# Kernel tuning notes

Measured on AMD Instinct MI355X. Metric: run time of the kernel, lower is better.

## Reference

```python
import jax, jax.numpy as jnp
import numpy as np

N_NODES = 50000
N_EDGES = 800000
IN_DIM = 128
OUT_DIM = 128
NEG_SLOPE = 0.01  # F.leaky_relu default


def setup_inputs() -> dict:
    key = jax.random.key(0)
    k_h, k_src, k_dst, k_w, k_as, k_ad = jax.random.split(key, 6)
    h = jax.random.normal(k_h, (N_NODES, IN_DIM), dtype=jnp.float32)
    src = jax.random.randint(k_src, (N_EDGES,), 0, N_NODES, dtype=jnp.int32)
    dst = jax.random.randint(k_dst, (N_EDGES,), 0, N_NODES, dtype=jnp.int32)
    # fc weight: xavier_normal with relu gain; stored as [in, out] for h @ W
    gain = float(np.sqrt(2.0))
    std_w = gain * np.sqrt(2.0 / (IN_DIM + OUT_DIM))
    W = jax.random.normal(k_w, (IN_DIM, OUT_DIM), dtype=jnp.float32) * std_w
    # attn weight [1, 2*out] split into src/dst halves (concat@a == z_s@a_s + z_d@a_d)
    std_a = gain * np.sqrt(2.0 / (2 * OUT_DIM + 1))
    a_src = jax.random.normal(k_as, (OUT_DIM,), dtype=jnp.float32) * std_a
    a_dst = jax.random.normal(k_ad, (OUT_DIM,), dtype=jnp.float32) * std_a
    return {"h": h, "src": src, "dst": dst, "W": W, "a_src": a_src, "a_dst": a_dst}


def reference(h, src, dst, W, a_src, a_dst):
    n = h.shape[0]
    z = h @ W                                   # [N, D]
    # edge attention: leaky_relu(attn(concat[z_src, z_dst]))
    e = z[src] @ a_src + z[dst] @ a_dst         # [E]
    e = jnp.where(e >= 0, e, NEG_SLOPE * e)
    # segment softmax over incoming edges of each dst node
    m = jax.ops.segment_max(e, dst, num_segments=n)    # [N]
    m = jnp.where(jnp.isfinite(m), m, 0.0)             # guard zero-in-degree nodes
    ex = jnp.exp(e - m[dst])                            # [E]
    denom = jax.ops.segment_sum(ex, dst, num_segments=n)
    denom = jnp.where(denom > 0, denom, 1.0)
    alpha = ex / denom[dst]                             # [E]
    # weighted scatter-sum of source features
    out = jax.ops.segment_sum(alpha[:, None] * z[src], dst, num_segments=n)  # [N, D]
    return out
```

## Files before the change

kernel.cpp:

```cpp
#include <hip/hip_runtime.h>
#include <math.h>

#define DIM 128
#define NEG_SLOPE 0.01f
#define CAP 64
#define NFILL 1024

typedef __attribute__((ext_vector_type(8))) short bf16x8;
typedef __attribute__((ext_vector_type(4))) float f32x4;
typedef unsigned int uint;
typedef unsigned short ushort;

static __device__ __forceinline__ uint f2bf(float x) {
  uint u = __float_as_uint(x);
  return (u + 0x7fffu + ((u >> 16) & 1u)) >> 16;
}

__global__ __launch_bounds__(256) void prep2(
    const float* __restrict__ W,
    const float* __restrict__ a_src, const float* __restrict__ a_dst,
    const float* __restrict__ h,
    ushort* __restrict__ Wt16, float* __restrict__ s, float* __restrict__ d,
    int* __restrict__ cur, int n, int nsd)
{
  const int t = threadIdx.x;
  const int b = blockIdx.x;
  if (b == 0) {
    const float4* W4 = (const float4*)W;
    #pragma unroll
    for (int it = 0; it < 16; ++it) {
      int i = t + it * 256;
      int k = i >> 5, n4 = (i & 31) * 4;
      float4 v = W4[i];
      Wt16[(n4 + 0) * 128 + k] = (ushort)f2bf(v.x);
      Wt16[(n4 + 1) * 128 + k] = (ushort)f2bf(v.y);
      Wt16[(n4 + 2) * 128 + k] = (ushort)f2bf(v.z);
      Wt16[(n4 + 3) * 128 + k] = (ushort)f2bf(v.w);
    }
  } else if (b <= nsd) {
    __shared__ float vec[2][DIM];
    {
      const float* row = W + (size_t)(t & 127) * DIM;
      const float* a = (t < 128) ? a_src : a_dst;
      float acc = 0.f;
      #pragma unroll 16
      for (int j = 0; j < DIM; ++j) acc = fmaf(row[j], a[j], acc);
      vec[t >> 7][t & 127] = acc;
    }
    __syncthreads();
    int i = (b - 1) * 256 + t;
    if (i < n) {
      const float4* h4 = (const float4*)(h + (size_t)i * DIM);
      float sp = 0.f, dp = 0.f;
      #pragma unroll 8
      for (int c = 0; c < 32; ++c) {
        float4 v = h4[c];
        sp = fmaf(v.x, vec[0][c*4+0], fmaf(v.y, vec[0][c*4+1],
             fmaf(v.z, vec[0][c*4+2], fmaf(v.w, vec[0][c*4+3], sp))));
        dp = fmaf(v.x, vec[1][c*4+0], fmaf(v.y, vec[1][c*4+1],
             fmaf(v.z, vec[1][c*4+2], fmaf(v.w, vec[1][c*4+3], dp))));
      }
      s[i] = sp; d[i] = dp;
    }
  } else {
    int i = (b - 1 - nsd) * 256 + t;
    if (i < n) cur[i] = i * CAP;
  }
}

__global__ __launch_bounds__(256) void gemm_mfma(
    const float* __restrict__ h, const ushort* __restrict__ Wt16,
    uint* __restrict__ zb,
    int n)
{
  __shared__ __align__(16) ushort hb[64 * 136];
  __shared__ __align__(16) ushort Wt[128 * 136];

  const int t = threadIdx.x;
  const int lane = t & 63, wv = t >> 6;
  const int row0 = blockIdx.x * 64;

  {
    const float4* h4 = (const float4*)h;
    #pragma unroll
    for (int it = 0; it < 8; ++it) {
      int i = t + it * 256;
      int r = i >> 5, c4 = i & 31;
      float4 v = make_float4(0.f, 0.f, 0.f, 0.f);
      if (row0 + r < n) v = h4[(size_t)(row0 + r) * 32 + c4];
      uint2 pk;
      pk.x = f2bf(v.x) | (f2bf(v.y) << 16);
      pk.y = f2bf(v.z) | (f2bf(v.w) << 16);
      *(uint2*)&hb[r * 136 + c4 * 4] = pk;
    }
  }
  {
    const uint4* Wg = (const uint4*)Wt16;
    #pragma unroll
    for (int it = 0; it < 8; ++it) {
      int i = t + it * 256;
      int nn = i >> 4, k8 = (i & 15) * 8;
      *(uint4*)&Wt[nn * 136 + k8] = Wg[i];
    }
  }
  __syncthreads();

  f32x4 acc[8];
  #pragma unroll
  for (int c = 0; c < 8; ++c) acc[c] = (f32x4){0.f, 0.f, 0.f, 0.f};

  const int m = lane & 15, quad = lane >> 4;
  const ushort* arow = &hb[(wv * 16 + m) * 136 + quad * 8];
  const ushort* brow = &Wt[m * 136 + quad * 8];

  #pragma unroll
  for (int ks = 0; ks < 4; ++ks) {
    bf16x8 af = *(const bf16x8*)(arow + ks * 32);
    #pragma unroll
    for (int c = 0; c < 8; ++c) {
      bf16x8 bf = *(const bf16x8*)(brow + c * 16 * 136 + ks * 32);
      acc[c] = __builtin_amdgcn_mfma_f32_16x16x32_bf16(af, bf, acc[c], 0, 0, 0);
    }
  }

  __syncthreads();
  #pragma unroll
  for (int c = 0; c < 8; ++c) {
    int col = c * 16 + m;
    #pragma unroll
    for (int reg = 0; reg < 4; ++reg) {
      int r = wv * 16 + quad * 4 + reg;
      hb[r * 136 + col] = (ushort)f2bf(acc[c][reg]);
    }
  }
  __syncthreads();
  #pragma unroll
  for (int it = 0; it < 4; ++it) {
    int i = t + it * 256;
    int r = i >> 4, c8 = i & 15;
    int rg = row0 + r;
    if (rg < n) {
      uint4 v = *(uint4*)&hb[r * 136 + c8 * 8];
      *(uint4*)&zb[(size_t)rg * 64 + c8 * 4] = v;
    }
  }
}

__global__ __launch_bounds__(256) void fill_bucket(
    const int* __restrict__ src, const int* __restrict__ dst,
    const float* __restrict__ s, const float* __restrict__ d,
    int* __restrict__ cur, uint* __restrict__ bucket, int E)
{
  const int base = blockIdx.x * 256 + threadIdx.x;
  const int stride = NFILL * 256;

  int idx[4]; bool ok[4];
  #pragma unroll
  for (int u = 0; u < 4; ++u) {
    int i = base + u * stride;
    ok[u] = (i < E);
    idx[u] = ok[u] ? i : 0;
  }
  int sj[4], dj[4];
  #pragma unroll
  for (int u = 0; u < 4; ++u) sj[u] = src[idx[u]];
  #pragma unroll
  for (int u = 0; u < 4; ++u) dj[u] = dst[idx[u]];
  float sv[4], dv[4];
  #pragma unroll
  for (int u = 0; u < 4; ++u) sv[u] = s[sj[u]];
  #pragma unroll
  for (int u = 0; u < 4; ++u) dv[u] = d[dj[u]];

  uint rec[4];
  #pragma unroll
  for (int u = 0; u < 4; ++u) {
    float e = sv[u] + dv[u];
    e = (e >= 0.f) ? e : NEG_SLOPE * e;
    rec[u] = (uint)sj[u] | (f2bf(__expf(e)) << 16);
  }
  int p[4];
  #pragma unroll
  for (int u = 0; u < 4; ++u)
    if (ok[u]) p[u] = atomicAdd(&cur[dj[u]], 1);
  #pragma unroll
  for (int u = 0; u < 4; ++u)
    if (ok[u] && p[u] < dj[u] * CAP + CAP)
      bucket[p[u]] = rec[u];
}

__global__ __launch_bounds__(256) void gat_node(
    const uint* __restrict__ zb, const int* __restrict__ cur,
    const uint* __restrict__ bucket, float* __restrict__ out, int n)
{
  int wave = threadIdx.x >> 6;
  int lane = threadIdx.x & 63;
  int node = blockIdx.x * 4 + wave;
  if (node >= n) return;

  int base = node * CAP;
  int cnt = min(cur[node] - base, CAP);
  float2* out2 = (float2*)out;
  if (cnt <= 0) {
    out2[(size_t)node * 64 + lane] = make_float2(0.f, 0.f);
    return;
  }

  uint rec = (lane < cnt) ? bucket[base + lane] : 0u;
  float denom = __uint_as_float(rec & 0xffff0000u);
  #pragma unroll
  for (int o = 32; o > 0; o >>= 1) denom += __shfl_xor(denom, o, 64);

  float2 acc = make_float2(0.f, 0.f);
  int tt = 0;
  for (; tt + 8 <= cnt; tt += 8) {
    uint rr[8], zv[8];
    #pragma unroll
    for (int u = 0; u < 8; ++u) {
      rr[u] = __shfl(rec, tt + u, 64);
      zv[u] = zb[(size_t)(rr[u] & 0xffffu) * 64 + lane];
    }
    #pragma unroll
    for (int u = 0; u < 8; ++u) {
      float wt = __uint_as_float(rr[u] & 0xffff0000u);
      acc.x = fmaf(wt, __uint_as_float(zv[u] << 16), acc.x);
      acc.y = fmaf(wt, __uint_as_float(zv[u] & 0xffff0000u), acc.y);
    }
  }
  for (; tt < cnt; ++tt) {
    uint r = __shfl(rec, tt, 64);
    uint u = zb[(size_t)(r & 0xffffu) * 64 + lane];
    float wt = __uint_as_float(r & 0xffff0000u);
    acc.x = fmaf(wt, __uint_as_float(u << 16), acc.x);
    acc.y = fmaf(wt, __uint_as_float(u & 0xffff0000u), acc.y);
  }
  float inv = 1.f / denom;
  out2[(size_t)node * 64 + lane] = make_float2(acc.x * inv, acc.y * inv);
}

extern "C" void kernel_launch(void* const* d_in, const int* in_sizes, int n_in,
                              void* d_out, int out_size, void* d_ws, size_t ws_size,
                              hipStream_t stream)
{
  const float* h     = (const float*)d_in[0];
  const int*   src   = (const int*)d_in[1];
  const int*   dst   = (const int*)d_in[2];
  const float* W     = (const float*)d_in[3];
  const float* a_src = (const float*)d_in[4];
  const float* a_dst = (const float*)d_in[5];
  float* out = (float*)d_out;

  const int n = in_sizes[0] / DIM;
  const int E = in_sizes[1];

  char* ws = (char*)d_ws;
  uint* zb     = (uint*)ws;   ws += (size_t)n * 64 * 4;
  float* s     = (float*)ws;  ws += (size_t)n * 4;
  float* d     = (float*)ws;  ws += (size_t)n * 4;
  int* cur     = (int*)ws;    ws += (size_t)n * 4;
  ushort* Wt16 = (ushort*)ws; ws += (size_t)DIM * DIM * 2;
  uint* bucket = (uint*)ws;

  const int nsd   = (n + 255) / 256;
  const int ncur  = (n + 255) / 256;
  const int ngemm = (n + 63) / 64;

  prep2<<<1 + nsd + ncur, 256, 0, stream>>>(W, a_src, a_dst, h, Wt16, s, d, cur, n, nsd);
  fill_bucket<<<NFILL, 256, 0, stream>>>(src, dst, s, d, cur, bucket, E);
  gemm_mfma<<<ngemm, 256, 0, stream>>>(h, Wt16, zb, n);
  gat_node<<<(n + 3) / 4, 256, 0, stream>>>(zb, cur, bucket, out, n);
}
```

Measured before the change: 183.1 us.

## Fuse edge bucketing into prep kernel and compute attention weights per node

Edge bucketing now runs inside the prep kernel, which stores only 16-bit source indices, and cur is zeroed with a memset instead of being initialised to bucket offsets. The per-edge attention score and exp move into the gather kernel, computed per lane from s and d. This drops one kernel launch and the dependency of bucketing on s and d, and halves bucket storage. In exchange the gather kernel does extra random reads of s and an exp per edge, adds a memset call, and 16-bit indices only hold when there are at most 65536 nodes.

Result: faster. 173.0 us (-5.5%).

```diff
diff --git a/kernel.cpp b/kernel.cpp
--- a/kernel.cpp
+++ b/kernel.cpp
@@ -4,7 +4,6 @@
 #define DIM 128
 #define NEG_SLOPE 0.01f
 #define CAP 64
-#define NFILL 1024
 
 typedef __attribute__((ext_vector_type(8))) short bf16x8;
 typedef __attribute__((ext_vector_type(4))) float f32x4;
@@ -16,15 +15,19 @@
   return (u + 0x7fffu + ((u >> 16) & 1u)) >> 16;
 }
 
-__global__ __launch_bounds__(256) void prep2(
+__global__ __launch_bounds__(256) void prep_fill(
     const float* __restrict__ W,
     const float* __restrict__ a_src, const float* __restrict__ a_dst,
     const float* __restrict__ h,
+    const int* __restrict__ src, const int* __restrict__ dst,
     ushort* __restrict__ Wt16, float* __restrict__ s, float* __restrict__ d,
-    int* __restrict__ cur, int n, int nsd)
-{
+    int* __restrict__ cur, ushort* __restrict__ bucket,
+    int n, int E, int nsd)
+{
+  __shared__ float vec[2][DIM];
   const int t = threadIdx.x;
   const int b = blockIdx.x;
+
   if (b == 0) {
     const float4* W4 = (const float4*)W;
     #pragma unroll
@@ -38,7 +41,6 @@
       Wt16[(n4 + 3) * 128 + k] = (ushort)f2bf(v.w);
     }
   } else if (b <= nsd) {
-    __shared__ float vec[2][DIM];
     {
       const float* row = W + (size_t)(t & 127) * DIM;
       const float* a = (t < 128) ? a_src : a_dst;
@@ -64,7 +66,12 @@
     }
   } else {
     int i = (b - 1 - nsd) * 256 + t;
-    if (i < n) cur[i] = i * CAP;
+    if (i < E) {
+      int sj = src[i], dj = dst[i];
+      int c = atomicAdd(&cur[dj], 1);
+      if (c < CAP)
+        bucket[dj * CAP + c] = (ushort)sj;
+    }
   }
 }
 
@@ -146,91 +153,55 @@
   }
 }
 
-__global__ __launch_bounds__(256) void fill_bucket(
-    const int* __restrict__ src, const int* __restrict__ dst,
-    const float* __restrict__ s, const float* __restrict__ d,
-    int* __restrict__ cur, uint* __restrict__ bucket, int E)
-{
-  const int base = blockIdx.x * 256 + threadIdx.x;
-  const int stride = NFILL * 256;
-
-  int idx[4]; bool ok[4];
-  #pragma unroll
-  for (int u = 0; u < 4; ++u) {
-    int i = base + u * stride;
-    ok[u] = (i < E);
-    idx[u] = ok[u] ? i : 0;
-  }
-  int sj[4], dj[4];
-  #pragma unroll
-  for (int u = 0; u < 4; ++u) sj[u] = src[idx[u]];
-  #pragma unroll
-  for (int u = 0; u < 4; ++u) dj[u] = dst[idx[u]];
-  float sv[4], dv[4];
-  #pragma unroll
-  for (int u = 0; u < 4; ++u) sv[u] = s[sj[u]];
-  #pragma unroll
-  for (int u = 0; u < 4; ++u) dv[u] = d[dj[u]];
-
-  uint rec[4];
-  #pragma unroll
-  for (int u = 0; u < 4; ++u) {
-    float e = sv[u] + dv[u];
-    e = (e >= 0.f) ? e : NEG_SLOPE * e;
-    rec[u] = (uint)sj[u] | (f2bf(__expf(e)) << 16);
-  }
-  int p[4];
-  #pragma unroll
-  for (int u = 0; u < 4; ++u)
-    if (ok[u]) p[u] = atomicAdd(&cur[dj[u]], 1);
-  #pragma unroll
-  for (int u = 0; u < 4; ++u)
-    if (ok[u] && p[u] < dj[u] * CAP + CAP)
-      bucket[p[u]] = rec[u];
-}
-
 __global__ __launch_bounds__(256) void gat_node(
-    const uint* __restrict__ zb, const int* __restrict__ cur,
-    const uint* __restrict__ bucket, float* __restrict__ out, int n)
+    const uint* __restrict__ zb, const float* __restrict__ s,
+    const float* __restrict__ d, const int* __restrict__ cur,
+    const ushort* __restrict__ bucket, float* __restrict__ out, int n)
 {
   int wave = threadIdx.x >> 6;
   int lane = threadIdx.x & 63;
   int node = blockIdx.x * 4 + wave;
   if (node >= n) return;
 
-  int base = node * CAP;
-  int cnt = min(cur[node] - base, CAP);
+  int cnt = min(cur[node], CAP);
   float2* out2 = (float2*)out;
   if (cnt <= 0) {
     out2[(size_t)node * 64 + lane] = make_float2(0.f, 0.f);
     return;
   }
 
-  uint rec = (lane < cnt) ? bucket[base + lane] : 0u;
-  float denom = __uint_as_float(rec & 0xffff0000u);
+  float dn = d[node];
+  int sj = 0; float w = 0.f;
+  if (lane < cnt) {
+    sj = (int)bucket[node * CAP + lane];
+    float e = s[sj] + dn;
+    e = (e >= 0.f) ? e : NEG_SLOPE * e;
+    w = __expf(e);
+  }
+  float denom = w;
   #pragma unroll
   for (int o = 32; o > 0; o >>= 1) denom += __shfl_xor(denom, o, 64);
 
   float2 acc = make_float2(0.f, 0.f);
   int tt = 0;
   for (; tt + 8 <= cnt; tt += 8) {
-    uint rr[8], zv[8];
+    uint zv[8]; float wt[8];
     #pragma unroll
     for (int u = 0; u < 8; ++u) {
-      rr[u] = __shfl(rec, tt + u, 64);
-      zv[u] = zb[(size_t)(rr[u] & 0xffffu) * 64 + lane];
+      int st = __shfl(sj, tt + u, 64);
+      zv[u] = zb[(size_t)st * 64 + lane];
+      wt[u] = __shfl(w, tt + u, 64);
     }
     #pragma unroll
     for (int u = 0; u < 8; ++u) {
-      float wt = __uint_as_float(rr[u] & 0xffff0000u);
-      acc.x = fmaf(wt, __uint_as_float(zv[u] << 16), acc.x);
-      acc.y = fmaf(wt, __uint_as_float(zv[u] & 0xffff0000u), acc.y);
+      acc.x = fmaf(wt[u], __uint_as_float(zv[u] << 16), acc.x);
+      acc.y = fmaf(wt[u], __uint_as_float(zv[u] & 0xffff0000u), acc.y);
     }
   }
   for (; tt < cnt; ++tt) {
-    uint r = __shfl(rec, tt, 64);
-    uint u = zb[(size_t)(r & 0xffffu) * 64 + lane];
-    float wt = __uint_as_float(r & 0xffff0000u);
+    int st = __shfl(sj, tt, 64);
+    uint u = zb[(size_t)st * 64 + lane];
+    float wt = __shfl(w, tt, 64);
     acc.x = fmaf(wt, __uint_as_float(u << 16), acc.x);
     acc.y = fmaf(wt, __uint_as_float(u & 0xffff0000u), acc.y);
   }
@@ -254,19 +225,20 @@
   const int E = in_sizes[1];
 
   char* ws = (char*)d_ws;
-  uint* zb     = (uint*)ws;   ws += (size_t)n * 64 * 4;
-  float* s     = (float*)ws;  ws += (size_t)n * 4;
-  float* d     = (float*)ws;  ws += (size_t)n * 4;
-  int* cur     = (int*)ws;    ws += (size_t)n * 4;
-  ushort* Wt16 = (ushort*)ws; ws += (size_t)DIM * DIM * 2;
-  uint* bucket = (uint*)ws;
+  uint* zb       = (uint*)ws;   ws += (size_t)n * 64 * 4;
+  float* s       = (float*)ws;  ws += (size_t)n * 4;
+  float* d       = (float*)ws;  ws += (size_t)n * 4;
+  int* cur       = (int*)ws;    ws += (size_t)n * 4;
+  ushort* Wt16   = (ushort*)ws; ws += (size_t)DIM * DIM * 2;
+  ushort* bucket = (ushort*)ws;
 
   const int nsd   = (n + 255) / 256;
-  const int ncur  = (n + 255) / 256;
+  const int nfill = (E + 255) / 256;
   const int ngemm = (n + 63) / 64;
 
-  prep2<<<1 + nsd + ncur, 256, 0, stream>>>(W, a_src, a_dst, h, Wt16, s, d, cur, n, nsd);
-  fill_bucket<<<NFILL, 256, 0, stream>>>(src, dst, s, d, cur, bucket, E);
+  hipMemsetAsync(cur, 0, (size_t)n * 4, stream);
+  prep_fill<<<1 + nsd + nfill, 256, 0, stream>>>(
+      W, a_src, a_dst, h, src, dst, Wt16, s, d, cur, bucket, n, E, nsd);
   gemm_mfma<<<ngemm, 256, 0, stream>>>(h, Wt16, zb, n);
-  gat_node<<<(n + 3) / 4, 256, 0, stream>>>(zb, cur, bucket, out, n);
-}
+  gat_node<<<(n + 3) / 4, 256, 0, stream>>>(zb, s, d, cur, bucket, out, n);
+}
```
